# Optimization experiments

Measured on AMD Instinct MI355X. Metric: run time of the kernel, lower is better.

## Reference

```python
import jax, jax.numpy as jnp
import numpy as np

B, C, D, H, W = 2, 128, 16, 96, 96


def setup_inputs() -> dict:
    key = jax.random.key(0)
    k1, k2 = jax.random.split(key)
    x = jax.random.normal(k1, (B, C, D, H, W), dtype=jnp.float32)
    gamma = jax.random.uniform(k2, (1,), dtype=jnp.float32)
    return {"x": x, "gamma": gamma}


def reference(x, gamma):
    b, c, d, h, w = x.shape
    n = d * h * w
    q = x.reshape(b, c, n)                      # [B,C,N] query==key==value
    # energy: [B,C,C] = q @ q^T
    energy = jnp.einsum('bcn,bdn->bcd', q, q)
    # EnergyMaxNorm: rowwise max (AdaptiveMaxPool1d(1) over last dim) minus energy
    e_max = jnp.max(energy, axis=-1, keepdims=True)
    energy = e_max - energy
    attn = jax.nn.softmax(energy, axis=-1)      # [B,C,C]
    out = jnp.einsum('bcd,bdn->bcn', attn, q)   # [B,C,N]
    out = out.reshape(b, c, d, h, w)
    # gamma-scaled residual fusion (modulation_type 'addition')
    return x + gamma[0] * out
```

## Files before the change

kernel.cpp:

```cpp
#include <hip/hip_runtime.h>

typedef unsigned short u16;
typedef unsigned int u32;
typedef __attribute__((ext_vector_type(8))) short short8;
typedef __attribute__((ext_vector_type(4))) float f32x4;
typedef __attribute__((ext_vector_type(4))) u16 u16x4;

#define NBATCH 2
#define NC 128
#define NN 147456
#define CH 64
#define NCH (NN / CH)
#define G1_PARTS 256
#define N3_PER_B 1152

__device__ __forceinline__ u16 bf16rne(float f) {
  u32 u = __builtin_bit_cast(u32, f);
  return (u16)((u + 0x7FFFu + ((u >> 16) & 1u)) >> 16);
}
__device__ __forceinline__ float bf2f(u16 h) {
  u32 u = ((u32)h) << 16;
  return __builtin_bit_cast(float, u);
}
__device__ __forceinline__ void split2(float f, u16& h, u16& g) {
  u32 u = __builtin_bit_cast(u32, f);
  h = (u16)(u >> 16);
  float hf = __builtin_bit_cast(float, u & 0xFFFF0000u);
  g = bf16rne(f - hf);
}

__global__ __launch_bounds__(256, 2)
void gram_k(const float* __restrict__ x, float* __restrict__ part) {
  __shared__ u16 hi[2][128 * CH];
  __shared__ u16 lo[2][128 * CH];
  const int tid = threadIdx.x;
  const int bid = blockIdx.x;
  const int b   = bid >> 8;
  const int pi  = bid & 255;
  const int w   = tid >> 6;
  const int l   = tid & 63;
  const int grp = l >> 4;
  const int lr  = l & 15;
  const int swz = (lr & 7) << 3;
  const float* xb = x + (size_t)b * NC * NN;

  const int col4 = tid & 15;
  const int r0   = tid >> 4;

  f32x4 acc[2][8];
#pragma unroll
  for (int i = 0; i < 2; ++i)
#pragma unroll
    for (int j = 0; j < 8; ++j) acc[i][j] = (f32x4){0.f, 0.f, 0.f, 0.f};

  float4 v[8];

  auto issue = [&](int ch) {
    const int k0 = ch * CH + (col4 << 2);
#pragma unroll
    for (int j = 0; j < 8; ++j)
      v[j] = *(const float4*)(xb + (size_t)(r0 + (j << 4)) * NN + k0);
  };
  auto stage = [&](int bb) {
    u16* H = &hi[bb][0];
    u16* L = &lo[bb][0];
#pragma unroll
    for (int j = 0; j < 8; ++j) {
      const int row = r0 + (j << 4);
      const int idx = (row << 6) + ((col4 << 2) ^ ((row & 7) << 3));
      u16 h0, h1, h2, h3, g0, g1, g2, g3;
      split2(v[j].x, h0, g0); split2(v[j].y, h1, g1);
      split2(v[j].z, h2, g2); split2(v[j].w, h3, g3);
      *(u16x4*)(H + idx) = (u16x4){h0, h1, h2, h3};
      *(u16x4*)(L + idx) = (u16x4){g0, g1, g2, g3};
    }
  };
  const int m0 = (w << 5) + lr;
  const int m1 = m0 + 16;
  auto mma = [&](int bb) {
    const u16* H = &hi[bb][0];
    const u16* L = &lo[bb][0];
#pragma unroll
    for (int kk = 0; kk < CH; kk += 32) {
      const int kv = (kk + (grp << 3)) ^ swz;
      const short8 Ah0 = *(const short8*)(H + (m0 << 6) + kv);
      const short8 Al0 = *(const short8*)(L + (m0 << 6) + kv);
      const short8 Ah1 = *(const short8*)(H + (m1 << 6) + kv);
      const short8 Al1 = *(const short8*)(L + (m1 << 6) + kv);
#pragma unroll
      for (int nt = 0; nt < 8; ++nt) {
        const int nr  = (nt << 4) + lr;
        const int bix = (nr << 6) + kv;
        const short8 Bh = *(const short8*)(H + bix);
        const short8 Bl = *(const short8*)(L + bix);
        acc[0][nt] = __builtin_amdgcn_mfma_f32_16x16x32_bf16(Ah0, Bh, acc[0][nt], 0, 0, 0);
        acc[0][nt] = __builtin_amdgcn_mfma_f32_16x16x32_bf16(Ah0, Bl, acc[0][nt], 0, 0, 0);
        acc[0][nt] = __builtin_amdgcn_mfma_f32_16x16x32_bf16(Al0, Bh, acc[0][nt], 0, 0, 0);
        acc[1][nt] = __builtin_amdgcn_mfma_f32_16x16x32_bf16(Ah1, Bh, acc[1][nt], 0, 0, 0);
        acc[1][nt] = __builtin_amdgcn_mfma_f32_16x16x32_bf16(Ah1, Bl, acc[1][nt], 0, 0, 0);
        acc[1][nt] = __builtin_amdgcn_mfma_f32_16x16x32_bf16(Al1, Bh, acc[1][nt], 0, 0, 0);
      }
    }
  };

  issue(pi);
  stage(0);
  __syncthreads();

  const int NITER = NCH / G1_PARTS;
  for (int i = 0; i < NITER; ++i) {
    if (i + 1 < NITER) issue(pi + (i + 1) * G1_PARTS);
    mma(i & 1);
    if (i + 1 < NITER) stage((i + 1) & 1);
    __syncthreads();
  }

  float* pb = part + (size_t)bid * 16384;
#pragma unroll
  for (int mt = 0; mt < 2; ++mt)
#pragma unroll
    for (int nt = 0; nt < 8; ++nt)
#pragma unroll
      for (int r = 0; r < 4; ++r) {
        const int row = (w << 5) + (mt << 4) + (grp << 2) + r;
        const int col = (nt << 4) + lr;
        pb[(row << 7) + col] = acc[mt][nt][r];
      }
}

__global__ __launch_bounds__(128)
void soft_k(const float* __restrict__ part, u16* __restrict__ attn) {
  const int b = blockIdx.x >> 7;
  const int c = blockIdx.x & 127;
  const int d = threadIdx.x;
  __shared__ float red[128];
  float e = 0.f;
  const float* p0 = part + ((size_t)(b * G1_PARTS) << 14) + (c << 7) + d;
  for (int p = 0; p < G1_PARTS; ++p) e += p0[(size_t)p << 14];
  red[d] = e;
  __syncthreads();
#pragma unroll
  for (int s = 64; s > 0; s >>= 1) {
    if (d < s) red[d] = fminf(red[d], red[d + s]);
    __syncthreads();
  }
  const float emin = red[0];
  __syncthreads();
  const float pr = __expf(emin - e);
  red[d] = pr;
  __syncthreads();
#pragma unroll
  for (int s = 64; s > 0; s >>= 1) {
    if (d < s) red[d] += red[d + s];
    __syncthreads();
  }
  const float inv = 1.f / red[0];
  attn[(((size_t)b) << 14) + (c << 7) + d] = bf16rne(pr * inv);
}

__global__ __launch_bounds__(256, 2)
void pv_k(const float* __restrict__ x, const u16* __restrict__ attn,
          const float* __restrict__ gamma, float* __restrict__ out) {
  __shared__ u16 at[128 * 128];
  const int tid = threadIdx.x;
  const int bid = blockIdx.x;
  const int b   = bid / N3_PER_B;
  const int nb  = (bid % N3_PER_B) << 7;
  const int w   = tid >> 6, l = tid & 63, grp = l >> 4, lr = l & 15;
  const int swz = lr << 3;
  const size_t bbase = (size_t)b * NC * NN;
  const u16* ab = attn + (((size_t)b) << 14);

#pragma unroll
  for (int j = 0; j < 8; ++j) {
    const int idx = (j << 8) + tid;
    const int c  = idx >> 4;
    const int d0 = (idx & 15) << 3;
    const int dst = (c << 7) + (d0 ^ ((c & 15) << 3));
    *(short8*)(at + dst) = *(const short8*)(ab + (c << 7) + d0);
  }
  __syncthreads();

  f32x4 acc[8][2];
#pragma unroll
  for (int i = 0; i < 8; ++i) {
    acc[i][0] = (f32x4){0.f, 0.f, 0.f, 0.f};
    acc[i][1] = (f32x4){0.f, 0.f, 0.f, 0.f};
  }

  const int n0 = nb + (w << 5) + lr;
#pragma unroll
  for (int kk = 0; kk < 128; kk += 32) {
    const int d0 = kk + (grp << 3);
    short8 Bh[2], Bl[2];
#pragma unroll
    for (int t = 0; t < 2; ++t) {
      const int n = n0 + (t << 4);
      const float* src = x + bbase + (size_t)d0 * NN + n;
      float f[8];
#pragma unroll
      for (int i = 0; i < 8; ++i) f[i] = src[(size_t)i * NN];
      u16 h[8], g[8];
#pragma unroll
      for (int i = 0; i < 8; ++i) {
        h[i] = bf16rne(f[i]);
        g[i] = bf16rne(f[i] - bf2f(h[i]));
      }
      Bh[t] = (short8){(short)h[0], (short)h[1], (short)h[2], (short)h[3],
                       (short)h[4], (short)h[5], (short)h[6], (short)h[7]};
      Bl[t] = (short8){(short)g[0], (short)g[1], (short)g[2], (short)g[3],
                       (short)g[4], (short)g[5], (short)g[6], (short)g[7]};
    }
#pragma unroll
    for (int mt = 0; mt < 8; ++mt) {
      const int mrow = (mt << 4) + lr;
      const short8 Ah = *(const short8*)(at + (mrow << 7) + ((kk + (grp << 3)) ^ swz));
#pragma unroll
      for (int t = 0; t < 2; ++t) {
        acc[mt][t] = __builtin_amdgcn_mfma_f32_16x16x32_bf16(Ah, Bh[t], acc[mt][t], 0, 0, 0);
        acc[mt][t] = __builtin_amdgcn_mfma_f32_16x16x32_bf16(Ah, Bl[t], acc[mt][t], 0, 0, 0);
      }
    }
  }

  const float gm = gamma[0];
#pragma unroll
  for (int mt = 0; mt < 8; ++mt)
#pragma unroll
    for (int t = 0; t < 2; ++t)
#pragma unroll
      for (int r = 0; r < 4; ++r) {
        const int c = (mt << 4) + (grp << 2) + r;
        const int n = n0 + (t << 4);
        const size_t off = bbase + (size_t)c * NN + n;
        out[off] = x[off] + gm * acc[mt][t][r];
      }
}

extern "C" void kernel_launch(void* const* d_in, const int* in_sizes, int n_in,
                              void* d_out, int out_size, void* d_ws, size_t ws_size,
                              hipStream_t stream) {
  (void)in_sizes; (void)n_in; (void)out_size; (void)ws_size;
  const float* x     = (const float*)d_in[0];
  const float* gamma = (const float*)d_in[1];
  float* out  = (float*)d_out;
  u16*   attn = (u16*)d_ws;
  float* part = out;

  gram_k<<<dim3(2 * G1_PARTS), dim3(256), 0, stream>>>(x, part);
  soft_k<<<dim3(2 * 128),      dim3(128), 0, stream>>>(part, attn);
  pv_k  <<<dim3(2 * N3_PER_B), dim3(256), 0, stream>>>(x, attn, gamma, out);
}
```

Measured before the change: 118.5 us.

## Stage x tile in LDS for PV kernel; read attention from global

The PV kernel now loads its 128x128 fp32 x tile with coalesced float4 global loads into swizzled shared memory, then builds the B operands from LDS instead of strided scalar global loads. The residual add also reads x from that tile rather than re-reading global memory. The attention matrix is no longer staged in LDS and is read directly from global (cache-resident) per k-step. LDS use doubles to 64KB per block, which may limit occupancy, and the swizzle indexing has to match on both the write and read side.

```diff
diff --git a/kernel.cpp b/kernel.cpp
--- a/kernel.cpp
+++ b/kernel.cpp
@@ -161,23 +161,29 @@
 __global__ __launch_bounds__(256, 2)
 void pv_k(const float* __restrict__ x, const u16* __restrict__ attn,
           const float* __restrict__ gamma, float* __restrict__ out) {
-  __shared__ u16 at[128 * 128];
+  __shared__ float xt[128 * 128];
   const int tid = threadIdx.x;
   const int bid = blockIdx.x;
   const int b   = bid / N3_PER_B;
   const int nb  = (bid % N3_PER_B) << 7;
-  const int w   = tid >> 6, l = tid & 63, grp = l >> 4, lr = l & 15;
-  const int swz = lr << 3;
+  const int w = tid >> 6, l = tid & 63, grp = l >> 4, lr = l & 15;
   const size_t bbase = (size_t)b * NC * NN;
-  const u16* ab = attn + (((size_t)b) << 14);
-
-#pragma unroll
-  for (int j = 0; j < 8; ++j) {
-    const int idx = (j << 8) + tid;
-    const int c  = idx >> 4;
-    const int d0 = (idx & 15) << 3;
-    const int dst = (c << 7) + (d0 ^ ((c & 15) << 3));
-    *(short8*)(at + dst) = *(const short8*)(ab + (c << 7) + d0);
+  const float* xb = x + bbase;
+  const u16* ab = attn + ((size_t)b << 14);
+
+  float4 sv[16];
+#pragma unroll
+  for (int j = 0; j < 16; ++j) {
+    const int f4  = tid + (j << 8);
+    const int row = f4 >> 5, fc = f4 & 31;
+    sv[j] = *(const float4*)(xb + (size_t)row * NN + nb + (fc << 2));
+  }
+#pragma unroll
+  for (int j = 0; j < 16; ++j) {
+    const int f4  = tid + (j << 8);
+    const int row = f4 >> 5, fc = f4 & 31;
+    const int fsw = fc ^ (((row >> 3) & 1) << 2);
+    *(float4*)(xt + (row << 7) + (fsw << 2)) = sv[j];
   }
   __syncthreads();
 
@@ -188,37 +194,35 @@
     acc[i][1] = (f32x4){0.f, 0.f, 0.f, 0.f};
   }
 
-  const int n0 = nb + (w << 5) + lr;
-#pragma unroll
-  for (int kk = 0; kk < 128; kk += 32) {
-    const int d0 = kk + (grp << 3);
-    short8 Bh[2], Bl[2];
+  const int nwt = (w << 5) + lr;
+
+#pragma unroll
+  for (int kk = 0; kk < 4; ++kk) {
+    const int KK = kk << 5;
+    short8 A[8];
+#pragma unroll
+    for (int mt = 0; mt < 8; ++mt)
+      A[mt] = *(const short8*)(ab + (((mt << 4) + lr) << 7) + KK + (grp << 3));
+
+    const int dbase = KK + (grp << 3);
 #pragma unroll
     for (int t = 0; t < 2; ++t) {
-      const int n = n0 + (t << 4);
-      const float* src = x + bbase + (size_t)d0 * NN + n;
+      const int nx = (nwt + (t << 4)) ^ ((grp & 1) << 4);
+      const float* bp = xt + (dbase << 7) + nx;
       float f[8];
 #pragma unroll
-      for (int i = 0; i < 8; ++i) f[i] = src[(size_t)i * NN];
+      for (int i = 0; i < 8; ++i) f[i] = bp[i << 7];
       u16 h[8], g[8];
 #pragma unroll
-      for (int i = 0; i < 8; ++i) {
-        h[i] = bf16rne(f[i]);
-        g[i] = bf16rne(f[i] - bf2f(h[i]));
-      }
-      Bh[t] = (short8){(short)h[0], (short)h[1], (short)h[2], (short)h[3],
-                       (short)h[4], (short)h[5], (short)h[6], (short)h[7]};
-      Bl[t] = (short8){(short)g[0], (short)g[1], (short)g[2], (short)g[3],
-                       (short)g[4], (short)g[5], (short)g[6], (short)g[7]};
-    }
-#pragma unroll
-    for (int mt = 0; mt < 8; ++mt) {
-      const int mrow = (mt << 4) + lr;
-      const short8 Ah = *(const short8*)(at + (mrow << 7) + ((kk + (grp << 3)) ^ swz));
-#pragma unroll
-      for (int t = 0; t < 2; ++t) {
-        acc[mt][t] = __builtin_amdgcn_mfma_f32_16x16x32_bf16(Ah, Bh[t], acc[mt][t], 0, 0, 0);
-        acc[mt][t] = __builtin_amdgcn_mfma_f32_16x16x32_bf16(Ah, Bl[t], acc[mt][t], 0, 0, 0);
+      for (int i = 0; i < 8; ++i) split2(f[i], h[i], g[i]);
+      const short8 Bh = (short8){(short)h[0], (short)h[1], (short)h[2], (short)h[3],
+                                 (short)h[4], (short)h[5], (short)h[6], (short)h[7]};
+      const short8 Bl = (short8){(short)g[0], (short)g[1], (short)g[2], (short)g[3],
+                                 (short)g[4], (short)g[5], (short)g[6], (short)g[7]};
+#pragma unroll
+      for (int mt = 0; mt < 8; ++mt) {
+        acc[mt][t] = __builtin_amdgcn_mfma_f32_16x16x32_bf16(A[mt], Bh, acc[mt][t], 0, 0, 0);
+        acc[mt][t] = __builtin_amdgcn_mfma_f32_16x16x32_bf16(A[mt], Bl, acc[mt][t], 0, 0, 0);
       }
     }
   }
@@ -231,9 +235,9 @@
 #pragma unroll
       for (int r = 0; r < 4; ++r) {
         const int c = (mt << 4) + (grp << 2) + r;
-        const int n = n0 + (t << 4);
-        const size_t off = bbase + (size_t)c * NN + n;
-        out[off] = x[off] + gm * acc[mt][t][r];
+        const int n = nwt + (t << 4);
+        const float rd = xt[(c << 7) + (n ^ ((grp >> 1) << 4))];
+        out[bbase + (size_t)c * NN + nb + n] = rd + gm * acc[mt][t][r];
       }
 }
 
```

Result: slower. 121.3 us (+2.3%).
